# Kernel tuning notes

Hardware: AMD Instinct MI355X
Metric: run time of the kernel (lower is better)

The kernel has to match this reference:

```python
import jax, jax.numpy as jnp
import numpy as np
from jax import lax

K = 5  # kernel size
D = 1  # dilation
CH = 32


def dw5(x, w, b, d=D):
    # depthwise 5x5 conv, NCHW, weight (C,1,5,5)
    y = lax.conv_general_dilated(
        x, w, window_strides=(1, 1), padding=[(2 * d, 2 * d), (2 * d, 2 * d)],
        rhs_dilation=(d, d), dimension_numbers=('NCHW', 'OIHW', 'NCHW'),
        feature_group_count=x.shape[1])
    return y + b[None, :, None, None]


def pw(x, w, b):
    # 1x1 conv, weight (O, C)
    return jnp.einsum('oc,nchw->nohw', w, x) + b[None, :, None, None]


def dynamic_dwconv(x, ksa, w, b, d=D):
    # involution-style dynamic depthwise conv (MyDepthWiseConv)
    # x: (n,c,h,wd); ksa: (n,K*K,h,wd); w: (c,K,K); b: (1,c,1,1)
    n, c, h, wd = x.shape
    pad = d * (K // 2)
    xp = jnp.pad(x, ((0, 0), (0, 0), (pad, pad), (pad, pad)))
    # patches (n,c,h,wd,K,K); kernel taps ordered row-major (i,j) to match nn.Unfold
    pats = jnp.stack(
        [xp[:, :, i * d:i * d + h, j * d:j * d + wd]
         for i in range(K) for j in range(K)], axis=-1).reshape(n, c, h, wd, K, K)
    # torch: (n,KK,h,w) -> (n,1,h,w,K,K); channel index = i*K + j (row-major)
    ksa_r = jnp.transpose(ksa, (0, 2, 3, 1)).reshape(n, h, wd, K, K)
    out = jnp.einsum('nchwkj,nhwkj,ckj->nchw', pats, ksa_r, w)
    return out + b


def cika_forward(lower, upper,
                 kca_dw_w, kca_dw_b, kca_m1_w, kca_m1_b, kca_m2_w, kca_m2_b,
                 ksa_dw_w, ksa_dw_b, ksa_m1_w, ksa_m1_b, ksa_m2_w, ksa_m2_b,
                 low_dyn_w, low_dyn_b, low_pw_w, low_pw_b,
                 up_dw_w, up_dw_b, up_pw_w, up_pw_b):
    # KCA(lower): depthwise5 -> relu -> 1x1 -> relu -> 1x1 -> sigmoid
    t = jax.nn.relu(dw5(lower, kca_dw_w, kca_dw_b))
    kca = jax.nn.sigmoid(pw(jax.nn.relu(pw(t, kca_m1_w, kca_m1_b)), kca_m2_w, kca_m2_b))
    # KSA(upper)
    t = jax.nn.relu(dw5(upper, ksa_dw_w, ksa_dw_b))
    ksa = jax.nn.sigmoid(pw(jax.nn.relu(pw(t, ksa_m1_w, ksa_m1_b)), ksa_m2_w, ksa_m2_b))
    # LowConv: dynamic depthwise then 1x1
    low = pw(dynamic_dwconv(lower, ksa, low_dyn_w, low_dyn_b), low_pw_w, low_pw_b)
    # UpConv: static depthwise, gate by kca, then 1x1
    up = pw(dw5(upper, up_dw_w, up_dw_b) * kca, up_pw_w, up_pw_b)
    return (low, up)


def setup_inputs() -> dict:
    key = jax.random.key(0)
    ks = jax.random.split(key, 24)
    N, C, H, W = 4, CH, 256, 256
    s = 0.1
    inp = {
        'lower': jax.random.normal(ks[0], (N, C, H, W), jnp.float32),
        'upper': jax.random.normal(ks[1], (N, C, H, W), jnp.float32),
        'kca_dw_w': jax.random.normal(ks[2], (C, 1, K, K), jnp.float32) * s,
        'kca_dw_b': jax.random.normal(ks[3], (C,), jnp.float32) * s,
        'kca_m1_w': jax.random.normal(ks[4], (C // 4, C), jnp.float32) * s,
        'kca_m1_b': jax.random.normal(ks[5], (C // 4,), jnp.float32) * s,
        'kca_m2_w': jax.random.normal(ks[6], (C, C // 4), jnp.float32) * s,
        'kca_m2_b': jax.random.normal(ks[7], (C,), jnp.float32) * s,
        'ksa_dw_w': jax.random.normal(ks[8], (C, 1, K, K), jnp.float32) * s,
        'ksa_dw_b': jax.random.normal(ks[9], (C,), jnp.float32) * s,
        'ksa_m1_w': jax.random.normal(ks[10], (2 * K * K, C), jnp.float32) * s,
        'ksa_m1_b': jax.random.normal(ks[11], (2 * K * K,), jnp.float32) * s,
        'ksa_m2_w': jax.random.normal(ks[12], (K * K, 2 * K * K), jnp.float32) * s,
        'ksa_m2_b': jax.random.normal(ks[13], (K * K,), jnp.float32) * s,
        'low_dyn_w': jax.random.normal(ks[14], (C, K, K), jnp.float32) * s,
        'low_dyn_b': jax.random.normal(ks[15], (1, C, 1, 1), jnp.float32) * s,
        'low_pw_w': jax.random.normal(ks[16], (C, C), jnp.float32) * s,
        'low_pw_b': jax.random.normal(ks[17], (C,), jnp.float32) * s,
        'up_dw_w': jax.random.normal(ks[18], (C, 1, K, K), jnp.float32) * s,
        'up_dw_b': jax.random.normal(ks[19], (C,), jnp.float32) * s,
        'up_pw_w': jax.random.normal(ks[20], (C, C), jnp.float32) * s,
        'up_pw_b': jax.random.normal(ks[21], (C,), jnp.float32) * s,
    }
    return inp


def reference(lower, upper,
              kca_dw_w, kca_dw_b, kca_m1_w, kca_m1_b, kca_m2_w, kca_m2_b,
              ksa_dw_w, ksa_dw_b, ksa_m1_w, ksa_m1_b, ksa_m2_w, ksa_m2_b,
              low_dyn_w, low_dyn_b, low_pw_w, low_pw_b,
              up_dw_w, up_dw_b, up_pw_w, up_pw_b):
    return cika_forward(lower, upper,
                        kca_dw_w, kca_dw_b, kca_m1_w, kca_m1_b, kca_m2_w, kca_m2_b,
                        ksa_dw_w, ksa_dw_b, ksa_m1_w, ksa_m1_b, ksa_m2_w, ksa_m2_b,
                        low_dyn_w, low_dyn_b, low_pw_w, low_pw_b,
                        up_dw_w, up_dw_b, up_pw_w, up_pw_b)
```

## Files before the change

kernel.cpp:

```cpp
#include <hip/hip_runtime.h>
#include <hip/hip_bf16.h>

#define KS 5
#define NCH 32
#define IMH 256
#define IMW 256
#define TW 32
#define TH 8
#define HALO_W (TW + 4)
#define HALO_H (TH + 4)
#define HW (IMH * IMW)
#define OC_CHUNK 8

#define CHUNK 4
#define NCHUNK (NCH / CHUNK)
#define TILE_ELEMS (CHUNK * HALO_H * HALO_W)
#define LOADS ((TILE_ELEMS + 255) / 256)

__device__ __forceinline__ float sigmoidf_(float x) {
    return 1.0f / (1.0f + __expf(-x));
}

__global__ __launch_bounds__(256) void cika_fused(
    const float* __restrict__ lower, const float* __restrict__ upper,
    const float* __restrict__ kca_dw_w, const float* __restrict__ kca_dw_b,
    const float* __restrict__ kca_m1_w, const float* __restrict__ kca_m1_b,
    const float* __restrict__ kca_m2_w, const float* __restrict__ kca_m2_b,
    const float* __restrict__ ksa_dw_w, const float* __restrict__ ksa_dw_b,
    const float* __restrict__ ksa_m1_w, const float* __restrict__ ksa_m1_b,
    const float* __restrict__ ksa_m2_w, const float* __restrict__ ksa_m2_b,
    const float* __restrict__ low_dyn_w, const float* __restrict__ low_dyn_b,
    const float* __restrict__ low_pw_w, const float* __restrict__ low_pw_b,
    const float* __restrict__ up_dw_w, const float* __restrict__ up_dw_b,
    const float* __restrict__ up_pw_w, const float* __restrict__ up_pw_b,
    float* __restrict__ out_low, float* __restrict__ out_up)
{
    __shared__ float tile[TILE_ELEMS];
    __shared__ __hip_bfloat16 dwk_td_lds[NCH][256];
    __shared__ __hip_bfloat16 dwu_lds[NCH][256];

    const int tid = threadIdx.x;
    const int tx = tid & (TW - 1);
    const int ty = tid >> 5;
    const int tile_x = blockIdx.x * TW;
    const int tile_y = blockIdx.y * TH;
    const int n = blockIdx.z;
    const int x = tile_x + tx, y = tile_y + ty;
    const int pix = y * IMW + x;

    const float* lob = lower + (size_t)n * NCH * HW;
    const float* upb = upper + (size_t)n * NCH * HW;

    int goff[LOADS];
    bool gok[LOADS];
    #pragma unroll
    for (int l = 0; l < LOADS; ++l) {
        const int idx = tid + l * 256;
        int c = idx / (HALO_H * HALO_W);
        int r = idx - c * (HALO_H * HALO_W);
        int hy = r / HALO_W, hx = r - hy * HALO_W;
        int gy = tile_y + hy - 2, gx = tile_x + hx - 2;
        gok[l] = (idx < TILE_ELEMS) && (gy >= 0) && (gy < IMH) && (gx >= 0) && (gx < IMW);
        goff[l] = c * HW + gy * IMW + gx;
    }

    {
        float pre[LOADS];
        #pragma unroll
        for (int l = 0; l < LOADS; ++l)
            pre[l] = gok[l] ? upb[(size_t)0 + goff[l]] : 0.0f;

        #pragma unroll 1
        for (int ck = 0; ck < NCHUNK; ++ck) {
            __syncthreads();
            #pragma unroll
            for (int l = 0; l < LOADS; ++l) {
                const int idx = tid + l * 256;
                if (idx < TILE_ELEMS) tile[idx] = pre[l];
            }
            __syncthreads();
            if (ck + 1 < NCHUNK) {
                const size_t base = (size_t)(ck + 1) * CHUNK * HW;
                #pragma unroll
                for (int l = 0; l < LOADS; ++l)
                    pre[l] = gok[l] ? upb[base + goff[l]] : 0.0f;
            }
            const int c0 = ck * CHUNK;
            #pragma unroll
            for (int cc = 0; cc < CHUNK; ++cc) {
                const int c = c0 + cc;
                float ak = ksa_dw_b[c];
                float au = up_dw_b[c];
                const float* tp = tile + cc * (HALO_H * HALO_W) + ty * HALO_W + tx;
                #pragma unroll
                for (int i = 0; i < KS; ++i)
                    #pragma unroll
                    for (int j = 0; j < KS; ++j) {
                        float wv = tp[i * HALO_W + j];
                        ak = fmaf(wv, ksa_dw_w[c * 25 + i * KS + j], ak);
                        au = fmaf(wv, up_dw_w[c * 25 + i * KS + j], au);
                    }
                dwk_td_lds[c][tid] = __float2bfloat16(fmaxf(ak, 0.0f));
                dwu_lds[c][tid]    = __float2bfloat16(au);
            }
        }
    }

    float ksa[25];
    {
        float dwk[NCH];
        #pragma unroll
        for (int c = 0; c < NCH; ++c)
            dwk[c] = __bfloat162float(dwk_td_lds[c][tid]);
        #pragma unroll
        for (int k = 0; k < 25; ++k) ksa[k] = ksa_m2_b[k];
        for (int h = 0; h < 50; ++h) {
            float hv = ksa_m1_b[h];
            #pragma unroll
            for (int c = 0; c < NCH; ++c)
                hv = fmaf(ksa_m1_w[h * NCH + c], dwk[c], hv);
            hv = fmaxf(hv, 0.0f);
            #pragma unroll
            for (int k = 0; k < 25; ++k)
                ksa[k] = fmaf(ksa_m2_w[k * 50 + h], hv, ksa[k]);
        }
        #pragma unroll
        for (int k = 0; k < 25; ++k) ksa[k] = sigmoidf_(ksa[k]);
    }

    float hv8[8];
    #pragma unroll
    for (int h = 0; h < 8; ++h) hv8[h] = kca_m1_b[h];
    {
        float pre[LOADS];
        #pragma unroll
        for (int l = 0; l < LOADS; ++l)
            pre[l] = gok[l] ? lob[(size_t)0 + goff[l]] : 0.0f;

        #pragma unroll 1
        for (int ck = 0; ck < NCHUNK; ++ck) {
            __syncthreads();
            #pragma unroll
            for (int l = 0; l < LOADS; ++l) {
                const int idx = tid + l * 256;
                if (idx < TILE_ELEMS) tile[idx] = pre[l];
            }
            __syncthreads();
            if (ck + 1 < NCHUNK) {
                const size_t base = (size_t)(ck + 1) * CHUNK * HW;
                #pragma unroll
                for (int l = 0; l < LOADS; ++l)
                    pre[l] = gok[l] ? lob[base + goff[l]] : 0.0f;
            }
            const int c0 = ck * CHUNK;
            #pragma unroll
            for (int cc = 0; cc < CHUNK; ++cc) {
                const int c = c0 + cc;
                float ad = kca_dw_b[c];
                float td = low_dyn_b[c];
                const float* tp = tile + cc * (HALO_H * HALO_W) + ty * HALO_W + tx;
                #pragma unroll
                for (int i = 0; i < KS; ++i)
                    #pragma unroll
                    for (int j = 0; j < KS; ++j) {
                        float wv = tp[i * HALO_W + j];
                        ad = fmaf(wv, kca_dw_w[c * 25 + i * KS + j], ad);
                        td = fmaf(wv * low_dyn_w[c * 25 + i * KS + j], ksa[i * KS + j], td);
                    }
                ad = fmaxf(ad, 0.0f);
                #pragma unroll
                for (int h = 0; h < 8; ++h)
                    hv8[h] = fmaf(kca_m1_w[h * NCH + c], ad, hv8[h]);
                dwk_td_lds[c][tid] = __float2bfloat16(td);
            }
        }
    }

    {
        float tdv[NCH];
        #pragma unroll
        for (int c = 0; c < NCH; ++c)
            tdv[c] = __bfloat162float(dwk_td_lds[c][tid]);
        float* ol = out_low + (size_t)n * NCH * HW + pix;
        #pragma unroll
        for (int oc = 0; oc < NCH / OC_CHUNK; ++oc) {
            float acc[OC_CHUNK];
            #pragma unroll
            for (int oo = 0; oo < OC_CHUNK; ++oo)
                acc[oo] = low_pw_b[oc * OC_CHUNK + oo];
            #pragma unroll
            for (int c = 0; c < NCH; ++c)
                #pragma unroll
                for (int oo = 0; oo < OC_CHUNK; ++oo)
                    acc[oo] = fmaf(low_pw_w[(oc * OC_CHUNK + oo) * NCH + c], tdv[c], acc[oo]);
            #pragma unroll
            for (int oo = 0; oo < OC_CHUNK; ++oo)
                ol[(size_t)(oc * OC_CHUNK + oo) * HW] = acc[oo];
        }
    }

    float kca[NCH];
    #pragma unroll
    for (int h = 0; h < 8; ++h) hv8[h] = fmaxf(hv8[h], 0.0f);
    #pragma unroll
    for (int k = 0; k < NCH; ++k) {
        float a = kca_m2_b[k];
        #pragma unroll
        for (int h = 0; h < 8; ++h)
            a = fmaf(kca_m2_w[k * 8 + h], hv8[h], a);
        kca[k] = sigmoidf_(a);
    }

    {
        float t2[NCH];
        #pragma unroll
        for (int c = 0; c < NCH; ++c)
            t2[c] = __bfloat162float(dwu_lds[c][tid]) * kca[c];
        float* ou = out_up + (size_t)n * NCH * HW + pix;
        #pragma unroll
        for (int oc = 0; oc < NCH / OC_CHUNK; ++oc) {
            float acc[OC_CHUNK];
            #pragma unroll
            for (int oo = 0; oo < OC_CHUNK; ++oo)
                acc[oo] = up_pw_b[oc * OC_CHUNK + oo];
            #pragma unroll
            for (int c = 0; c < NCH; ++c)
                #pragma unroll
                for (int oo = 0; oo < OC_CHUNK; ++oo)
                    acc[oo] = fmaf(up_pw_w[(oc * OC_CHUNK + oo) * NCH + c], t2[c], acc[oo]);
            #pragma unroll
            for (int oo = 0; oo < OC_CHUNK; ++oo)
                ou[(size_t)(oc * OC_CHUNK + oo) * HW] = acc[oo];
        }
    }
}

extern "C" void kernel_launch(void* const* d_in, const int* in_sizes, int n_in,
                              void* d_out, int out_size, void* d_ws, size_t ws_size,
                              hipStream_t stream) {
    const float* lower    = (const float*)d_in[0];
    const float* upper    = (const float*)d_in[1];
    const float* kca_dw_w = (const float*)d_in[2];
    const float* kca_dw_b = (const float*)d_in[3];
    const float* kca_m1_w = (const float*)d_in[4];
    const float* kca_m1_b = (const float*)d_in[5];
    const float* kca_m2_w = (const float*)d_in[6];
    const float* kca_m2_b = (const float*)d_in[7];
    const float* ksa_dw_w = (const float*)d_in[8];
    const float* ksa_dw_b = (const float*)d_in[9];
    const float* ksa_m1_w = (const float*)d_in[10];
    const float* ksa_m1_b = (const float*)d_in[11];
    const float* ksa_m2_w = (const float*)d_in[12];
    const float* ksa_m2_b = (const float*)d_in[13];
    const float* low_dyn_w = (const float*)d_in[14];
    const float* low_dyn_b = (const float*)d_in[15];
    const float* low_pw_w  = (const float*)d_in[16];
    const float* low_pw_b  = (const float*)d_in[17];
    const float* up_dw_w   = (const float*)d_in[18];
    const float* up_dw_b   = (const float*)d_in[19];
    const float* up_pw_w   = (const float*)d_in[20];
    const float* up_pw_b   = (const float*)d_in[21];

    const int N = in_sizes[0] / (NCH * HW);
    float* out_low = (float*)d_out;
    float* out_up  = (float*)d_out + (size_t)N * NCH * HW;

    dim3 grid(IMW / TW, IMH / TH, N);
    cika_fused<<<grid, dim3(256), 0, stream>>>(
        lower, upper,
        kca_dw_w, kca_dw_b, kca_m1_w, kca_m1_b, kca_m2_w, kca_m2_b,
        ksa_dw_w, ksa_dw_b, ksa_m1_w, ksa_m1_b, ksa_m2_w, ksa_m2_b,
        low_dyn_w, low_dyn_b, low_pw_w, low_pw_b,
        up_dw_w, up_dw_b, up_pw_w, up_pw_b,
        out_low, out_up);
}
```

Baseline: 114.6 us.

## Split channels across two thread groups with half-height tiles

Tile height is halved so each 256-thread block covers 128 pixels with two thread groups. Each group handles half the channels in the depthwise stages and half the output channels in the pointwise stages. The KCA hidden partial sums are combined between the groups through LDS. The goal is more blocks and more parallelism per pixel, but both groups recompute the full KSA MLP for the same pixel, and the halo-to-tile ratio grows.

```diff
diff --git a/kernel.cpp b/kernel.cpp
--- a/kernel.cpp
+++ b/kernel.cpp
@@ -6,15 +6,17 @@
 #define IMH 256
 #define IMW 256
 #define TW 32
-#define TH 8
+#define TH 4
 #define HALO_W (TW + 4)
 #define HALO_H (TH + 4)
 #define HW (IMH * IMW)
+#define NPIX 128
 #define OC_CHUNK 8
 
-#define CHUNK 4
-#define NCHUNK (NCH / CHUNK)
-#define TILE_ELEMS (CHUNK * HALO_H * HALO_W)
+#define SLOTS 4
+#define NCHUNK 8
+#define SLOT_SZ (HALO_H * HALO_W)
+#define TILE_ELEMS (SLOTS * SLOT_SZ)
 #define LOADS ((TILE_ELEMS + 255) / 256)
 
 __device__ __forceinline__ float sigmoidf_(float x) {
@@ -36,12 +38,14 @@
     float* __restrict__ out_low, float* __restrict__ out_up)
 {
     __shared__ float tile[TILE_ELEMS];
-    __shared__ __hip_bfloat16 dwk_td_lds[NCH][256];
-    __shared__ __hip_bfloat16 dwu_lds[NCH][256];
+    __shared__ __hip_bfloat16 dwk_td_lds[NCH][NPIX];
+    __shared__ __hip_bfloat16 dwu_lds[NCH][NPIX];
 
     const int tid = threadIdx.x;
-    const int tx = tid & (TW - 1);
-    const int ty = tid >> 5;
+    const int g   = tid >> 7;
+    const int s   = tid & (NPIX - 1);
+    const int tx  = s & (TW - 1);
+    const int ty  = s >> 5;
     const int tile_x = blockIdx.x * TW;
     const int tile_y = blockIdx.y * TH;
     const int n = blockIdx.z;
@@ -56,19 +60,20 @@
     #pragma unroll
     for (int l = 0; l < LOADS; ++l) {
         const int idx = tid + l * 256;
-        int c = idx / (HALO_H * HALO_W);
-        int r = idx - c * (HALO_H * HALO_W);
+        int sl = idx / SLOT_SZ;
+        int r  = idx - sl * SLOT_SZ;
         int hy = r / HALO_W, hx = r - hy * HALO_W;
         int gy = tile_y + hy - 2, gx = tile_x + hx - 2;
+        int cbase = (sl < 2) ? sl : (14 + sl);
         gok[l] = (idx < TILE_ELEMS) && (gy >= 0) && (gy < IMH) && (gx >= 0) && (gx < IMW);
-        goff[l] = c * HW + gy * IMW + gx;
+        goff[l] = cbase * HW + gy * IMW + gx;
     }
 
     {
         float pre[LOADS];
         #pragma unroll
         for (int l = 0; l < LOADS; ++l)
-            pre[l] = gok[l] ? upb[(size_t)0 + goff[l]] : 0.0f;
+            pre[l] = gok[l] ? upb[(size_t)goff[l]] : 0.0f;
 
         #pragma unroll 1
         for (int ck = 0; ck < NCHUNK; ++ck) {
@@ -80,18 +85,18 @@
             }
             __syncthreads();
             if (ck + 1 < NCHUNK) {
-                const size_t base = (size_t)(ck + 1) * CHUNK * HW;
+                const size_t base = (size_t)(ck + 1) * 2 * HW;
                 #pragma unroll
                 for (int l = 0; l < LOADS; ++l)
                     pre[l] = gok[l] ? upb[base + goff[l]] : 0.0f;
             }
-            const int c0 = ck * CHUNK;
-            #pragma unroll
-            for (int cc = 0; cc < CHUNK; ++cc) {
-                const int c = c0 + cc;
+            #pragma unroll
+            for (int cc = 0; cc < 2; ++cc) {
+                const int c  = g * 16 + 2 * ck + cc;
+                const int sl = g * 2 + cc;
                 float ak = ksa_dw_b[c];
                 float au = up_dw_b[c];
-                const float* tp = tile + cc * (HALO_H * HALO_W) + ty * HALO_W + tx;
+                const float* tp = tile + sl * SLOT_SZ + ty * HALO_W + tx;
                 #pragma unroll
                 for (int i = 0; i < KS; ++i)
                     #pragma unroll
@@ -100,18 +105,19 @@
                         ak = fmaf(wv, ksa_dw_w[c * 25 + i * KS + j], ak);
                         au = fmaf(wv, up_dw_w[c * 25 + i * KS + j], au);
                     }
-                dwk_td_lds[c][tid] = __float2bfloat16(fmaxf(ak, 0.0f));
-                dwu_lds[c][tid]    = __float2bfloat16(au);
-            }
-        }
-    }
+                dwk_td_lds[c][s] = __float2bfloat16(fmaxf(ak, 0.0f));
+                dwu_lds[c][s]    = __float2bfloat16(au);
+            }
+        }
+    }
+    __syncthreads();
 
     float ksa[25];
     {
         float dwk[NCH];
         #pragma unroll
         for (int c = 0; c < NCH; ++c)
-            dwk[c] = __bfloat162float(dwk_td_lds[c][tid]);
+            dwk[c] = __bfloat162float(dwk_td_lds[c][s]);
         #pragma unroll
         for (int k = 0; k < 25; ++k) ksa[k] = ksa_m2_b[k];
         for (int h = 0; h < 50; ++h) {
@@ -130,12 +136,13 @@
 
     float hv8[8];
     #pragma unroll
-    for (int h = 0; h < 8; ++h) hv8[h] = kca_m1_b[h];
+    for (int h = 0; h < 8; ++h)
+        hv8[h] = (g == 0) ? kca_m1_b[h] : 0.0f;
     {
         float pre[LOADS];
         #pragma unroll
         for (int l = 0; l < LOADS; ++l)
-            pre[l] = gok[l] ? lob[(size_t)0 + goff[l]] : 0.0f;
+            pre[l] = gok[l] ? lob[(size_t)goff[l]] : 0.0f;
 
         #pragma unroll 1
         for (int ck = 0; ck < NCHUNK; ++ck) {
@@ -147,18 +154,18 @@
             }
             __syncthreads();
             if (ck + 1 < NCHUNK) {
-                const size_t base = (size_t)(ck + 1) * CHUNK * HW;
+                const size_t base = (size_t)(ck + 1) * 2 * HW;
                 #pragma unroll
                 for (int l = 0; l < LOADS; ++l)
                     pre[l] = gok[l] ? lob[base + goff[l]] : 0.0f;
             }
-            const int c0 = ck * CHUNK;
-            #pragma unroll
-            for (int cc = 0; cc < CHUNK; ++cc) {
-                const int c = c0 + cc;
+            #pragma unroll
+            for (int cc = 0; cc < 2; ++cc) {
+                const int c  = g * 16 + 2 * ck + cc;
+                const int sl = g * 2 + cc;
                 float ad = kca_dw_b[c];
                 float td = low_dyn_b[c];
-                const float* tp = tile + cc * (HALO_H * HALO_W) + ty * HALO_W + tx;
+                const float* tp = tile + sl * SLOT_SZ + ty * HALO_W + tx;
                 #pragma unroll
                 for (int i = 0; i < KS; ++i)
                     #pragma unroll
@@ -171,66 +178,78 @@
                 #pragma unroll
                 for (int h = 0; h < 8; ++h)
                     hv8[h] = fmaf(kca_m1_w[h * NCH + c], ad, hv8[h]);
-                dwk_td_lds[c][tid] = __float2bfloat16(td);
-            }
-        }
-    }
+                dwk_td_lds[c][s] = __float2bfloat16(td);
+            }
+        }
+    }
+    __syncthreads();
 
     {
         float tdv[NCH];
         #pragma unroll
         for (int c = 0; c < NCH; ++c)
-            tdv[c] = __bfloat162float(dwk_td_lds[c][tid]);
+            tdv[c] = __bfloat162float(dwk_td_lds[c][s]);
         float* ol = out_low + (size_t)n * NCH * HW + pix;
         #pragma unroll
-        for (int oc = 0; oc < NCH / OC_CHUNK; ++oc) {
+        for (int og = 0; og < 2; ++og) {
+            const int ob = g * 16 + og * OC_CHUNK;
             float acc[OC_CHUNK];
             #pragma unroll
             for (int oo = 0; oo < OC_CHUNK; ++oo)
-                acc[oo] = low_pw_b[oc * OC_CHUNK + oo];
+                acc[oo] = low_pw_b[ob + oo];
             #pragma unroll
             for (int c = 0; c < NCH; ++c)
                 #pragma unroll
                 for (int oo = 0; oo < OC_CHUNK; ++oo)
-                    acc[oo] = fmaf(low_pw_w[(oc * OC_CHUNK + oo) * NCH + c], tdv[c], acc[oo]);
-            #pragma unroll
-            for (int oo = 0; oo < OC_CHUNK; ++oo)
-                ol[(size_t)(oc * OC_CHUNK + oo) * HW] = acc[oo];
-        }
-    }
+                    acc[oo] = fmaf(low_pw_w[(ob + oo) * NCH + c], tdv[c], acc[oo]);
+            #pragma unroll
+            for (int oo = 0; oo < OC_CHUNK; ++oo)
+                ol[(size_t)(ob + oo) * HW] = acc[oo];
+        }
+    }
+    __syncthreads();
 
     float kca[NCH];
-    #pragma unroll
-    for (int h = 0; h < 8; ++h) hv8[h] = fmaxf(hv8[h], 0.0f);
-    #pragma unroll
-    for (int k = 0; k < NCH; ++k) {
-        float a = kca_m2_b[k];
+    {
+        __hip_bfloat16* hvp = &dwk_td_lds[0][0];
         #pragma unroll
         for (int h = 0; h < 8; ++h)
-            a = fmaf(kca_m2_w[k * 8 + h], hv8[h], a);
-        kca[k] = sigmoidf_(a);
+            hvp[h * 256 + tid] = __float2bfloat16(hv8[h]);
+        __syncthreads();
+        #pragma unroll
+        for (int h = 0; h < 8; ++h)
+            hv8[h] = fmaxf(hv8[h] + __bfloat162float(hvp[h * 256 + (tid ^ 128)]), 0.0f);
+        #pragma unroll
+        for (int k = 0; k < NCH; ++k) {
+            float a = kca_m2_b[k];
+            #pragma unroll
+            for (int h = 0; h < 8; ++h)
+                a = fmaf(kca_m2_w[k * 8 + h], hv8[h], a);
+            kca[k] = sigmoidf_(a);
+        }
     }
 
     {
         float t2[NCH];
         #pragma unroll
         for (int c = 0; c < NCH; ++c)
-            t2[c] = __bfloat162float(dwu_lds[c][tid]) * kca[c];
+            t2[c] = __bfloat162float(dwu_lds[c][s]) * kca[c];
         float* ou = out_up + (size_t)n * NCH * HW + pix;
         #pragma unroll
-        for (int oc = 0; oc < NCH / OC_CHUNK; ++oc) {
+        for (int og = 0; og < 2; ++og) {
+            const int ob = g * 16 + og * OC_CHUNK;
             float acc[OC_CHUNK];
             #pragma unroll
             for (int oo = 0; oo < OC_CHUNK; ++oo)
-                acc[oo] = up_pw_b[oc * OC_CHUNK + oo];
+                acc[oo] = up_pw_b[ob + oo];
             #pragma unroll
             for (int c = 0; c < NCH; ++c)
                 #pragma unroll
                 for (int oo = 0; oo < OC_CHUNK; ++oo)
-                    acc[oo] = fmaf(up_pw_w[(oc * OC_CHUNK + oo) * NCH + c], t2[c], acc[oo]);
-            #pragma unroll
-            for (int oo = 0; oo < OC_CHUNK; ++oo)
-                ou[(size_t)(oc * OC_CHUNK + oo) * HW] = acc[oo];
+                    acc[oo] = fmaf(up_pw_w[(ob + oo) * NCH + c], t2[c], acc[oo]);
+            #pragma unroll
+            for (int oo = 0; oo < OC_CHUNK; ++oo)
+                ou[(size_t)(ob + oo) * HW] = acc[oo];
         }
     }
 }
```

Result: slower. 241.2 us (+110.4%).
